# Kernel tuning notes

Hardware: AMD Instinct MI355X
Metric: run time of the kernel (lower is better)

## Reference

```python
import jax, jax.numpy as jnp
import numpy as np

# dims
N, K, M = 16000, 16, 20000      # nodes, neighbors per node, expanded (out-cell) nodes
C = 128                          # TP value channels = num_attn_heads * head_dim = scalar_dim
H = 8                            # num_attn_heads
LMAX = 2
L2 = (LMAX + 1) ** 2             # 9 spherical components
CE, CH = 64, 128                 # edge feature dim, radial MLP hidden
SD = 128                         # scalar_dim (irreps_node_input[0][0])


def _layer_norm(x, g, b, eps=1e-5):
    mu = jnp.mean(x, axis=-1, keepdims=True)
    var = jnp.var(x, axis=-1, keepdims=True)
    return (x - mu) * jax.lax.rsqrt(var + eps) * g + b


def setup_inputs() -> dict:
    key = jax.random.key(0)
    ks = jax.random.split(key, 20)
    f32 = jnp.float32
    return {
        "alpha": jax.random.normal(ks[0], (N, K, H), f32),
        "value": jax.random.normal(ks[1], (N, L2, C), f32) * 0.1,
        "x_edge": jax.random.normal(ks[2], (N, K, CE), f32),
        "node_pos": jax.random.normal(ks[3], (N, 3), f32) * 3.0,
        "edge_dis": jax.random.uniform(ks[4], (N, K), f32, 0.5, 4.5),
        "exp_node_pos": jax.random.normal(ks[5], (M, 3), f32) * 3.0,
        # radial MLP (RadialFunction: Linear -> LayerNorm -> SiLU -> Linear)
        "rad_w1": jax.random.normal(ks[6], (CE, CH), f32) / np.sqrt(CE),
        "rad_b1": jnp.zeros((CH,), f32),
        "ln_g": jnp.ones((CH,), f32),
        "ln_b": jnp.zeros((CH,), f32),
        "rad_w2": jax.random.normal(ks[7], (CH, SD), f32) / np.sqrt(CH),
        "rad_b2": jnp.zeros((SD,), f32),
        # uvw-connected first-order tensor-product weights (channel mixing per path)
        "tp_w_same": jax.random.normal(ks[8], (LMAX + 1, C, C), f32) / np.sqrt(C),
        "tp_w_rv0": jax.random.normal(ks[9], (C, C), f32) / np.sqrt(C),
        "tp_w_rdot": jax.random.normal(ks[10], (C, C), f32) / np.sqrt(C),
        # SO3 linear projection (per-degree linear, bias only on l=0)
        "proj_w": jax.random.normal(ks[11], (LMAX + 1, C, SD), f32) / np.sqrt(C),
        "proj_b": jnp.zeros((SD,), f32),
        # int index tensors
        "outcell_index": jax.random.randint(ks[12], (M,), 0, N, jnp.int32),
        "f_sparse_idx_expnode": jax.random.randint(ks[13], (N, K), 0, M, jnp.int32),
    }


def reference(alpha, value, x_edge, node_pos, edge_dis, exp_node_pos,
              rad_w1, rad_b1, ln_g, ln_b, rad_w2, rad_b2,
              tp_w_same, tp_w_rv0, tp_w_rdot, proj_w, proj_b,
              outcell_index, f_sparse_idx_expnode):
    # --- radial gating of attention weights ---
    h = jax.nn.silu(_layer_norm(x_edge @ rad_w1 + rad_b1, ln_g, ln_b))
    inputhead = h @ rad_w2 + rad_b2                          # [N,K,SD]
    n, k = alpha.shape[0], alpha.shape[1]
    a = alpha.reshape(n, k, H, 1) * inputhead.reshape(n, k, H, SD // H)
    a = a.reshape(n, k, SD)                                  # [N,K,C] (SD == C)
    a = a / (edge_dis[..., None] + 1e-8)

    # --- sparse equivariant first-order tensor product ---
    v_exp = value[outcell_index]                             # [M,L2,C]
    V = v_exp[f_sparse_idx_expnode]                          # [N,K,L2,C] (dominant gather)
    r = node_pos[:, None, :] - exp_node_pos[f_sparse_idx_expnode]  # [N,K,3]

    aV = jnp.einsum('nkc,nklc->nlc', a, V)                   # same-degree aggregation
    rv0 = a * V[:, :, 0, :]                                  # [N,K,C]
    arV0 = jnp.einsum('nkx,nkc->nxc', r, rv0)                # l=0 (x) r -> l=1
    wv1 = a[:, :, None, :] * V[:, :, 1:4, :]                 # [N,K,3,C]
    ardot = jnp.einsum('nkx,nkxc->nc', r, wv1)               # l=1 (x) r -> l=0

    out0 = aV[:, 0, :] @ tp_w_same[0] + ardot @ tp_w_rdot    # [N,C]
    out1 = jnp.einsum('nxc,cd->nxd', aV[:, 1:4, :], tp_w_same[1]) \
         + jnp.einsum('nxc,cd->nxd', arV0, tp_w_rv0)         # [N,3,C]
    out2 = jnp.einsum('nmc,cd->nmd', aV[:, 4:9, :], tp_w_same[2])  # [N,5,C]
    tp_out = jnp.concatenate([out0[:, None, :], out1, out2], axis=1)  # [N,9,C]

    # --- SO3 linear projection (per-degree) ---
    y0 = tp_out[:, 0, :] @ proj_w[0] + proj_b                # bias only on l=0
    y1 = jnp.einsum('nxc,cd->nxd', tp_out[:, 1:4, :], proj_w[1])
    y2 = jnp.einsum('nmc,cd->nmd', tp_out[:, 4:9, :], proj_w[2])
    return jnp.concatenate([y0[:, None, :], y1, y2], axis=1)  # [N,9,SD]
```

## Files before the change

### kernel.cpp

```cpp
#include <hip/hip_runtime.h>
#include <hip/hip_fp16.h>

typedef __attribute__((ext_vector_type(8))) short bh8;
typedef __attribute__((ext_vector_type(4))) float fv4;

#define NB 8
#define EB 128
#define BLK 512

#define MFMA(a, b, c) __builtin_amdgcn_mfma_f32_16x16x32_bf16((a), (b), (c), 0, 0, 0)

__device__ __forceinline__ unsigned short f2bf(float x) {
    unsigned int u = __float_as_uint(x);
    u += 0x7fffu + ((u >> 16) & 1u);
    return (unsigned short)(u >> 16);
}
__device__ __forceinline__ float bf2f(unsigned short h) {
    return __uint_as_float(((unsigned int)h) << 16);
}
__device__ __forceinline__ int swz(int row, int col) {
    return row * 128 + ((((col >> 3) ^ (row & 7)) << 3) | (col & 7));
}

__global__ void prep_kernel(
    const float* __restrict__ rad_w1, const float* __restrict__ rad_w2,
    const float* __restrict__ tp_w_same, const float* __restrict__ tp_w_rv0,
    const float* __restrict__ tp_w_rdot, const float* __restrict__ proj_w,
    unsigned short* __restrict__ ws)
{
    unsigned short* w1T = ws;
    unsigned short* w2T = ws + 8192;
    unsigned short* wcF = ws + 24576;
    const int b = blockIdx.x, t = threadIdx.x;
    if (b < 640) {
        const int m = b >> 7, d = b & 127;
        const float* A; const float* B;
        if (m == 0)      { A = tp_w_same;         B = proj_w; }
        else if (m == 1) { A = tp_w_rdot;         B = proj_w; }
        else if (m == 2) { A = tp_w_same + 16384; B = proj_w + 16384; }
        else if (m == 3) { A = tp_w_rv0;          B = proj_w + 16384; }
        else             { A = tp_w_same + 32768; B = proj_w + 32768; }
        __shared__ float Bs[128];
        Bs[t] = B[t * 128 + d];
        __syncthreads();
        float acc = 0.f;
        const float* Ar = A + t * 128;
        #pragma unroll 4
        for (int x = 0; x < 128; ++x) acc = fmaf(Ar[x], Bs[x], acc);
        const int wt = d >> 4, l15 = d & 15;
        const int ks = t >> 5, lq = (t & 31) >> 3, j = t & 7;
        const int lane = l15 + 16 * lq;
        wcF[(((m * 8 + wt) * 4 + ks) << 9) + lane * 8 + j] = f2bf(acc);
    } else {
        const int bb = b - 640;
        #pragma unroll
        for (int i = 0; i < 12; ++i) {
            const int idx = bb * 1536 + i * 128 + t;
            if (idx < 8192) {
                const int j = idx >> 6, c = idx & 63;
                w1T[idx] = f2bf(rad_w1[c * 128 + j]);
            } else if (idx < 24576) {
                const int i2 = idx - 8192;
                const int j = i2 >> 7, c = i2 & 127;
                w2T[i2] = f2bf(rad_w2[c * 128 + j]);
            }
        }
    }
}

__global__ __launch_bounds__(256) void conv_value_kernel(
    const float* __restrict__ v, unsigned short* __restrict__ o, int n8)
{
    const int i = blockIdx.x * 256 + threadIdx.x;
    if (i >= n8) return;
    const float4 a = *(const float4*)(v + (size_t)i * 8);
    const float4 b = *(const float4*)(v + (size_t)i * 8 + 4);
    uint4 r;
    r.x = (unsigned int)__half_as_ushort(__float2half_rn(a.x)) |
          ((unsigned int)__half_as_ushort(__float2half_rn(a.y)) << 16);
    r.y = (unsigned int)__half_as_ushort(__float2half_rn(a.z)) |
          ((unsigned int)__half_as_ushort(__float2half_rn(a.w)) << 16);
    r.z = (unsigned int)__half_as_ushort(__float2half_rn(b.x)) |
          ((unsigned int)__half_as_ushort(__float2half_rn(b.y)) << 16);
    r.w = (unsigned int)__half_as_ushort(__float2half_rn(b.z)) |
          ((unsigned int)__half_as_ushort(__float2half_rn(b.w)) << 16);
    *(uint4*)(o + (size_t)i * 8) = r;
}

template <int VHALF>
__global__ __launch_bounds__(BLK, 4) void foa_main(
    const float* __restrict__ alpha,
    const float* __restrict__ value,
    const float* __restrict__ x_edge,
    const float* __restrict__ node_pos,
    const float* __restrict__ edge_dis,
    const float* __restrict__ exp_node_pos,
    const float* __restrict__ rad_b1, const float* __restrict__ ln_g,
    const float* __restrict__ ln_b, const float* __restrict__ rad_b2,
    const float* __restrict__ proj_b,
    const unsigned short* __restrict__ ws,
    const unsigned short* __restrict__ vhf,
    const int* __restrict__ outcell_index,
    const int* __restrict__ f_sparse_idx,
    float* __restrict__ out)
{
    __shared__ __align__(16) unsigned short s_buf[16384];
    __shared__ __align__(16) unsigned short s_w2[16384];
    __shared__ float s_alpha[1024];
    __shared__ float s_rE[EB][3];
    __shared__ float s_invd[EB];
    __shared__ int   s_gidx[EB];

    const unsigned short* w1T = ws;
    const unsigned short* w2T = ws + 8192;
    const unsigned short* wcF = ws + 24576;

    const int t = threadIdx.x;
    const int e0 = blockIdx.x * EB;
    const int n0 = blockIdx.x * NB;
    const int lane = t & 63, w = t >> 6;
    const int ln15 = lane & 15, lq = lane >> 4;

    if (t < EB) {
        const int eidx = f_sparse_idx[e0 + t];
        s_gidx[t] = outcell_index[eidx];
        const int nn = n0 + (t >> 4);
        s_rE[t][0] = node_pos[nn * 3 + 0] - exp_node_pos[(size_t)eidx * 3 + 0];
        s_rE[t][1] = node_pos[nn * 3 + 1] - exp_node_pos[(size_t)eidx * 3 + 1];
        s_rE[t][2] = node_pos[nn * 3 + 2] - exp_node_pos[(size_t)eidx * 3 + 2];
        s_invd[t] = 1.0f / (edge_dis[e0 + t] + 1e-8f);
    }
    s_alpha[t]       = alpha[(size_t)e0 * 8 + t];
    s_alpha[t + 512] = alpha[(size_t)e0 * 8 + 512 + t];
    #pragma unroll
    for (int i = 0; i < 2; ++i) {
        const int chunk = i * BLK + t;
        const int row = chunk >> 3, grp = chunk & 7;
        const bh8 v = *(const bh8*)&w1T[row * 64 + grp * 8];
        *(bh8*)&s_w2[row * 64 + ((grp ^ (row & 7)) << 3)] = v;
    }
    __syncthreads();

    {
        bh8 af0, af1;
        {
            const float* xp = x_edge + ((size_t)(e0 + 16 * w + ln15)) * 64 + lq * 8;
            const float4 u0 = *(const float4*)(xp);
            const float4 u1 = *(const float4*)(xp + 4);
            const float4 u2 = *(const float4*)(xp + 32);
            const float4 u3 = *(const float4*)(xp + 36);
            af0[0] = (short)f2bf(u0.x); af0[1] = (short)f2bf(u0.y);
            af0[2] = (short)f2bf(u0.z); af0[3] = (short)f2bf(u0.w);
            af0[4] = (short)f2bf(u1.x); af0[5] = (short)f2bf(u1.y);
            af0[6] = (short)f2bf(u1.z); af0[7] = (short)f2bf(u1.w);
            af1[0] = (short)f2bf(u2.x); af1[1] = (short)f2bf(u2.y);
            af1[2] = (short)f2bf(u2.z); af1[3] = (short)f2bf(u2.w);
            af1[4] = (short)f2bf(u3.x); af1[5] = (short)f2bf(u3.y);
            af1[6] = (short)f2bf(u3.z); af1[7] = (short)f2bf(u3.w);
        }
        fv4 acc1[8];
        #pragma unroll
        for (int ct = 0; ct < 8; ++ct) { fv4 z = {0.f, 0.f, 0.f, 0.f}; acc1[ct] = z; }
        #pragma unroll
        for (int ct = 0; ct < 8; ++ct) {
            const int brow = 16 * ct + ln15;
            const bh8 b0 = *(const bh8*)&s_w2[brow * 64 + ((lq ^ (brow & 7)) << 3)];
            const bh8 b1 = *(const bh8*)&s_w2[brow * 64 + (((lq + 4) ^ (brow & 7)) << 3)];
            acc1[ct] = MFMA(af0, b0, acc1[ct]);
            acc1[ct] = MFMA(af1, b1, acc1[ct]);
        }
        float b1v[8], gv[8], bvv[8];
        #pragma unroll
        for (int ct = 0; ct < 8; ++ct) {
            b1v[ct] = rad_b1[16 * ct + ln15];
            gv[ct]  = ln_g[16 * ct + ln15];
            bvv[ct] = ln_b[16 * ct + ln15];
        }
        #pragma unroll
        for (int r = 0; r < 4; ++r) {
            float vv[8], s = 0.f, s2 = 0.f;
            #pragma unroll
            for (int ct = 0; ct < 8; ++ct) {
                const float x = acc1[ct][r] + b1v[ct];
                vv[ct] = x; s += x; s2 += x * x;
            }
            s += __shfl_xor(s, 1);  s2 += __shfl_xor(s2, 1);
            s += __shfl_xor(s, 2);  s2 += __shfl_xor(s2, 2);
            s += __shfl_xor(s, 4);  s2 += __shfl_xor(s2, 4);
            s += __shfl_xor(s, 8);  s2 += __shfl_xor(s2, 8);
            const float mu = s * 0.0078125f;
            const float var = s2 * 0.0078125f - mu * mu;
            const float rstd = rsqrtf(var + 1e-5f);
            const int rowg = 16 * w + lq * 4 + r;
            #pragma unroll
            for (int ct = 0; ct < 8; ++ct) {
                float hh = (vv[ct] - mu) * rstd * gv[ct] + bvv[ct];
                hh = hh / (1.f + __expf(-hh));
                s_buf[swz(rowg, 16 * ct + ln15)] = f2bf(hh);
            }
        }
    }
    __syncthreads();

    #pragma unroll
    for (int i = 0; i < 4; ++i) {
        const int chunk = i * BLK + t;
        const int row = chunk >> 4, grp = chunk & 15;
        const bh8 v = *(const bh8*)&w2T[row * 128 + grp * 8];
        *(bh8*)&s_w2[row * 128 + ((grp ^ (row & 7)) << 3)] = v;
    }
    __syncthreads();

    {
        bh8 afr[4];
        const int arow = 16 * w + ln15;
        #pragma unroll
        for (int ks = 0; ks < 4; ++ks) {
            const int acb = (lq + 4 * ks) ^ (arow & 7);
            afr[ks] = *(const bh8*)&s_buf[arow * 128 + (acb << 3)];
        }
        fv4 acc2[8];
        #pragma unroll
        for (int ct = 0; ct < 8; ++ct) { fv4 z = {0.f, 0.f, 0.f, 0.f}; acc2[ct] = z; }
        #pragma unroll
        for (int ks = 0; ks < 4; ++ks) {
            #pragma unroll
            for (int ct = 0; ct < 8; ++ct) {
                const int brow = 16 * ct + ln15;
                const bh8 b = *(const bh8*)&s_w2[brow * 128 +
                                  (((lq + 4 * ks) ^ (brow & 7)) << 3)];
                acc2[ct] = MFMA(afr[ks], b, acc2[ct]);
            }
        }
        #pragma unroll
        for (int ct = 0; ct < 8; ++ct) {
            const float b2 = rad_b2[16 * ct + ln15];
            #pragma unroll
            for (int r = 0; r < 4; ++r) {
                const int e = 16 * w + lq * 4 + r;
                const float aval = s_alpha[e * 8 + ct] * (acc2[ct][r] + b2) * s_invd[e];
                s_buf[swz(e, 16 * ct + ln15)] = f2bf(aval);
            }
        }
    }
    __syncthreads();

    const int c = t & 127;
    const int ng = t >> 7;
    float aV[9], arr[3], ard;

    #pragma unroll
    for (int ep = 0; ep < 2; ++ep) {
        #pragma unroll
        for (int l = 0; l < 9; ++l) aV[l] = 0.f;
        arr[0] = 0.f; arr[1] = 0.f; arr[2] = 0.f; ard = 0.f;
        #pragma unroll 4
        for (int k = 0; k < 16; ++k) {
            const int e = 32 * ng + 16 * ep + k;
            const float av = bf2f(s_buf[swz(e, c)]);
            float v0, v1, v2, v3, v4, v5, v6, v7, v8;
            if constexpr (VHALF) {
                const __half* vp = (const __half*)vhf + (size_t)s_gidx[e] * 1152 + c;
                v0 = __half2float(vp[0]);    v1 = __half2float(vp[128]);
                v2 = __half2float(vp[256]);  v3 = __half2float(vp[384]);
                v4 = __half2float(vp[512]);  v5 = __half2float(vp[640]);
                v6 = __half2float(vp[768]);  v7 = __half2float(vp[896]);
                v8 = __half2float(vp[1024]);
            } else {
                const float* vp = value + (size_t)s_gidx[e] * 1152 + c;
                v0 = vp[0];    v1 = vp[128];  v2 = vp[256];
                v3 = vp[384];  v4 = vp[512];  v5 = vp[640];
                v6 = vp[768];  v7 = vp[896];  v8 = vp[1024];
            }
            aV[0] = fmaf(av, v0, aV[0]); aV[1] = fmaf(av, v1, aV[1]);
            aV[2] = fmaf(av, v2, aV[2]); aV[3] = fmaf(av, v3, aV[3]);
            aV[4] = fmaf(av, v4, aV[4]); aV[5] = fmaf(av, v5, aV[5]);
            aV[6] = fmaf(av, v6, aV[6]); aV[7] = fmaf(av, v7, aV[7]);
            aV[8] = fmaf(av, v8, aV[8]);
            const float r0 = s_rE[e][0], r1 = s_rE[e][1], r2 = s_rE[e][2];
            const float w0 = av * v0;
            arr[0] = fmaf(r0, w0, arr[0]);
            arr[1] = fmaf(r1, w0, arr[1]);
            arr[2] = fmaf(r2, w0, arr[2]);
            ard = fmaf(av, fmaf(r0, v1, fmaf(r1, v2, r2 * v3)), ard);
        }
        __syncthreads();
        const int rb = 16 * ep;
        s_buf[swz(rb + 0  + ng, c)] = f2bf(aV[0]);
        s_buf[swz(rb + 4  + ng, c)] = f2bf(aV[1]);
        s_buf[swz(rb + 8  + ng, c)] = f2bf(aV[2]);
        s_buf[swz(rb + 12 + ng, c)] = f2bf(aV[3]);
        s_buf[swz(rb + 32 + ng, c)] = f2bf(ard);
        s_buf[swz(rb + 36 + ng, c)] = f2bf(arr[0]);
        s_buf[swz(rb + 40 + ng, c)] = f2bf(arr[1]);
        s_buf[swz(rb + 44 + ng, c)] = f2bf(arr[2]);
        s_buf[swz(rb + 64 + ng, c)] = f2bf(aV[4]);
        s_buf[swz(rb + 68 + ng, c)] = f2bf(aV[5]);
        s_buf[swz(rb + 72 + ng, c)] = f2bf(aV[6]);
        s_buf[swz(rb + 76 + ng, c)] = f2bf(aV[7]);
        s_buf[swz(96 + 4 * ep + ng, c)] = f2bf(aV[8]);
    }
    __syncthreads();

    {
        fv4 aEA, aEB, aEC, aOA, aOB, aOC, aG;
        { fv4 z = {0.f,0.f,0.f,0.f}; aEA=z; aEB=z; aEC=z; aOA=z; aOB=z; aOC=z; aG=z; }
        #pragma unroll
        for (int ks = 0; ks < 4; ++ks) {
            const int cb = lq + 4 * ks;
        #define LDA(tb) (*(const bh8*)&s_buf[((tb) + ln15) * 128 + (((cb) ^ (((tb) + ln15) & 7)) << 3)])
        #define LDB(m)  (*(const bh8*)&wcF[((((m) * 8 + w) * 4 + ks) << 9) + lane * 8])
            const bh8 W0 = LDB(0), Wd = LDB(1), W1 = LDB(2), Wr = LDB(3), W2 = LDB(4);
            const bh8 A0 = LDA(0),  A2 = LDA(32);
            aEA = MFMA(A0, W0, aEA);  aEA = MFMA(A2, Wd, aEA);
            aEB = MFMA(A0, W1, aEB);  aEB = MFMA(A2, Wr, aEB);
            const bh8 A1 = LDA(16), A3 = LDA(48);
            aOA = MFMA(A1, W0, aOA);  aOA = MFMA(A3, Wd, aOA);
            aOB = MFMA(A1, W1, aOB);  aOB = MFMA(A3, Wr, aOB);
            aEC = MFMA(LDA(64), W2, aEC);
            aOC = MFMA(LDA(80), W2, aOC);
            aG  = MFMA(LDA(96), W2, aG);
        #undef LDA
        #undef LDB
        }
        const int d = 16 * w + ln15;
        const float pb = proj_b[d];
        float* ob = out + (size_t)n0 * 1152 + d;
        #pragma unroll
        for (int r = 0; r < 4; ++r) {
            const int rt = lq * 4 + r;
            const int s = rt & 3;
            {
                const int l4 = 4 + (rt >> 2);
                ob[(size_t)(2 * s) * 1152 + l4 * 128]     = aEC[r];
                ob[(size_t)(2 * s + 1) * 1152 + l4 * 128] = aOC[r];
            }
            if (rt < 4) {
                ob[(size_t)(2 * rt) * 1152]             = aEA[r] + pb;
                ob[(size_t)(2 * rt + 1) * 1152]         = aOA[r] + pb;
                ob[(size_t)(2 * rt) * 1152 + 8 * 128]   = aG[r];
            } else {
                const int l = rt >> 2;
                ob[(size_t)(2 * s) * 1152 + l * 128]     = aEB[r];
                ob[(size_t)(2 * s + 1) * 1152 + l * 128] = aOB[r];
                if (rt < 8)
                    ob[(size_t)(2 * (rt - 4) + 1) * 1152 + 8 * 128] = aG[r];
            }
        }
    }
}

extern "C" void kernel_launch(void* const* d_in, const int* in_sizes, int n_in,
                              void* d_out, int out_size, void* d_ws, size_t ws_size,
                              hipStream_t stream)
{
    const float* alpha        = (const float*)d_in[0];
    const float* value        = (const float*)d_in[1];
    const float* x_edge       = (const float*)d_in[2];
    const float* node_pos     = (const float*)d_in[3];
    const float* edge_dis     = (const float*)d_in[4];
    const float* exp_node_pos = (const float*)d_in[5];
    const float* rad_w1       = (const float*)d_in[6];
    const float* rad_b1       = (const float*)d_in[7];
    const float* ln_g         = (const float*)d_in[8];
    const float* ln_b         = (const float*)d_in[9];
    const float* rad_w2       = (const float*)d_in[10];
    const float* rad_b2       = (const float*)d_in[11];
    const float* tp_w_same    = (const float*)d_in[12];
    const float* tp_w_rv0     = (const float*)d_in[13];
    const float* tp_w_rdot    = (const float*)d_in[14];
    const float* proj_w       = (const float*)d_in[15];
    const float* proj_b       = (const float*)d_in[16];
    const int* outcell_index  = (const int*)d_in[17];
    const int* f_sparse_idx   = (const int*)d_in[18];
    float* out = (float*)d_out;
    unsigned short* ws = (unsigned short*)d_ws;

    const int N = in_sizes[0] / (16 * 8);
    const int vElems = in_sizes[1];

    prep_kernel<<<656, 128, 0, stream>>>(rad_w1, rad_w2, tp_w_same, tp_w_rv0,
                                         tp_w_rdot, proj_w, ws);

    const size_t need = ((size_t)106496 + (size_t)vElems) * 2;
    if (ws_size >= need) {
        unsigned short* vhf = ws + 106496;
        const int n8 = vElems / 8;
        conv_value_kernel<<<(n8 + 255) / 256, 256, 0, stream>>>(value, vhf, n8);
        foa_main<1><<<N / NB, BLK, 0, stream>>>(alpha, value, x_edge, node_pos, edge_dis,
                                                exp_node_pos, rad_b1, ln_g, ln_b, rad_b2,
                                                proj_b, ws, vhf, outcell_index,
                                                f_sparse_idx, out);
    } else {
        foa_main<0><<<N / NB, BLK, 0, stream>>>(alpha, value, x_edge, node_pos, edge_dis,
                                                exp_node_pos, rad_b1, ln_g, ln_b, rad_b2,
                                                proj_b, ws, ws, outcell_index,
                                                f_sparse_idx, out);
    }
}
```

Before: 152.1 us.

## Pack fp16 value pairs into 32-bit words and hoist x_edge loads

The fp16 value conversion now interleaves pairs of spherical components per channel into 32-bit words, 640 words per node with the last component padded. The main kernel's gather then issues five loads per edge instead of nine and unpacks them with half2-to-float2 conversion. Separately, the x_edge fragment load and bf16 conversion are moved ahead of the shared-memory setup and the first barrier, so that global latency overlaps with the setup. The packed layout needs somewhat more workspace because of the padding, and the earlier load keeps those registers live longer.

```diff
diff --git a/kernel.cpp b/kernel.cpp
--- a/kernel.cpp
+++ b/kernel.cpp
@@ -68,23 +68,23 @@
     }
 }
 
-__global__ __launch_bounds__(256) void conv_value_kernel(
-    const float* __restrict__ v, unsigned short* __restrict__ o, int n8)
+__global__ __launch_bounds__(128) void conv_value_p_kernel(
+    const float* __restrict__ v, unsigned int* __restrict__ o)
 {
-    const int i = blockIdx.x * 256 + threadIdx.x;
-    if (i >= n8) return;
-    const float4 a = *(const float4*)(v + (size_t)i * 8);
-    const float4 b = *(const float4*)(v + (size_t)i * 8 + 4);
-    uint4 r;
-    r.x = (unsigned int)__half_as_ushort(__float2half_rn(a.x)) |
-          ((unsigned int)__half_as_ushort(__float2half_rn(a.y)) << 16);
-    r.y = (unsigned int)__half_as_ushort(__float2half_rn(a.z)) |
-          ((unsigned int)__half_as_ushort(__float2half_rn(a.w)) << 16);
-    r.z = (unsigned int)__half_as_ushort(__float2half_rn(b.x)) |
-          ((unsigned int)__half_as_ushort(__float2half_rn(b.y)) << 16);
-    r.w = (unsigned int)__half_as_ushort(__float2half_rn(b.z)) |
-          ((unsigned int)__half_as_ushort(__float2half_rn(b.w)) << 16);
-    *(uint4*)(o + (size_t)i * 8) = r;
+    const int n = blockIdx.x;
+    const int c = threadIdx.x;
+    const float* vp = v + (size_t)n * 1152 + c;
+    float x[9];
+    #pragma unroll
+    for (int l = 0; l < 9; ++l) x[l] = vp[l * 128];
+    unsigned int* op = o + (size_t)n * 640 + c;
+    #pragma unroll
+    for (int lp = 0; lp < 4; ++lp) {
+        const unsigned int lo = __half_as_ushort(__float2half_rn(x[2 * lp]));
+        const unsigned int hi = __half_as_ushort(__float2half_rn(x[2 * lp + 1]));
+        op[lp * 128] = lo | (hi << 16);
+    }
+    op[512] = (unsigned int)__half_as_ushort(__float2half_rn(x[8]));
 }
 
 template <int VHALF>
@@ -99,7 +99,7 @@
     const float* __restrict__ ln_b, const float* __restrict__ rad_b2,
     const float* __restrict__ proj_b,
     const unsigned short* __restrict__ ws,
-    const unsigned short* __restrict__ vhf,
+    const unsigned int* __restrict__ vhp,
     const int* __restrict__ outcell_index,
     const int* __restrict__ f_sparse_idx,
     float* __restrict__ out)
@@ -121,6 +121,22 @@
     const int lane = t & 63, w = t >> 6;
     const int ln15 = lane & 15, lq = lane >> 4;
 
+    bh8 af0, af1;
+    {
+        const float* xp = x_edge + ((size_t)(e0 + 16 * w + ln15)) * 64 + lq * 8;
+        const float4 u0 = *(const float4*)(xp);
+        const float4 u1 = *(const float4*)(xp + 4);
+        const float4 u2 = *(const float4*)(xp + 32);
+        const float4 u3 = *(const float4*)(xp + 36);
+        af0[0] = (short)f2bf(u0.x); af0[1] = (short)f2bf(u0.y);
+        af0[2] = (short)f2bf(u0.z); af0[3] = (short)f2bf(u0.w);
+        af0[4] = (short)f2bf(u1.x); af0[5] = (short)f2bf(u1.y);
+        af0[6] = (short)f2bf(u1.z); af0[7] = (short)f2bf(u1.w);
+        af1[0] = (short)f2bf(u2.x); af1[1] = (short)f2bf(u2.y);
+        af1[2] = (short)f2bf(u2.z); af1[3] = (short)f2bf(u2.w);
+        af1[4] = (short)f2bf(u3.x); af1[5] = (short)f2bf(u3.y);
+        af1[6] = (short)f2bf(u3.z); af1[7] = (short)f2bf(u3.w);
+    }
     if (t < EB) {
         const int eidx = f_sparse_idx[e0 + t];
         s_gidx[t] = outcell_index[eidx];
@@ -142,22 +158,6 @@
     __syncthreads();
 
     {
-        bh8 af0, af1;
-        {
-            const float* xp = x_edge + ((size_t)(e0 + 16 * w + ln15)) * 64 + lq * 8;
-            const float4 u0 = *(const float4*)(xp);
-            const float4 u1 = *(const float4*)(xp + 4);
-            const float4 u2 = *(const float4*)(xp + 32);
-            const float4 u3 = *(const float4*)(xp + 36);
-            af0[0] = (short)f2bf(u0.x); af0[1] = (short)f2bf(u0.y);
-            af0[2] = (short)f2bf(u0.z); af0[3] = (short)f2bf(u0.w);
-            af0[4] = (short)f2bf(u1.x); af0[5] = (short)f2bf(u1.y);
-            af0[6] = (short)f2bf(u1.z); af0[7] = (short)f2bf(u1.w);
-            af1[0] = (short)f2bf(u2.x); af1[1] = (short)f2bf(u2.y);
-            af1[2] = (short)f2bf(u2.z); af1[3] = (short)f2bf(u2.w);
-            af1[4] = (short)f2bf(u3.x); af1[5] = (short)f2bf(u3.y);
-            af1[6] = (short)f2bf(u3.z); af1[7] = (short)f2bf(u3.w);
-        }
         fv4 acc1[8];
         #pragma unroll
         for (int ct = 0; ct < 8; ++ct) { fv4 z = {0.f, 0.f, 0.f, 0.f}; acc1[ct] = z; }
@@ -260,12 +260,19 @@
             const float av = bf2f(s_buf[swz(e, c)]);
             float v0, v1, v2, v3, v4, v5, v6, v7, v8;
             if constexpr (VHALF) {
-                const __half* vp = (const __half*)vhf + (size_t)s_gidx[e] * 1152 + c;
-                v0 = __half2float(vp[0]);    v1 = __half2float(vp[128]);
-                v2 = __half2float(vp[256]);  v3 = __half2float(vp[384]);
-                v4 = __half2float(vp[512]);  v5 = __half2float(vp[640]);
-                v6 = __half2float(vp[768]);  v7 = __half2float(vp[896]);
-                v8 = __half2float(vp[1024]);
+                const unsigned int* vp = vhp + (size_t)s_gidx[e] * 640 + c;
+                const unsigned int q0 = vp[0];
+                const unsigned int q1 = vp[128];
+                const unsigned int q2 = vp[256];
+                const unsigned int q3 = vp[384];
+                const unsigned short q4 = *(const unsigned short*)(vp + 512);
+                const float2 f0 = __half22float2(*(const __half2*)&q0);
+                const float2 f1 = __half22float2(*(const __half2*)&q1);
+                const float2 f2 = __half22float2(*(const __half2*)&q2);
+                const float2 f3 = __half22float2(*(const __half2*)&q3);
+                v0 = f0.x; v1 = f0.y; v2 = f1.x; v3 = f1.y;
+                v4 = f2.x; v5 = f2.y; v6 = f3.x; v7 = f3.y;
+                v8 = __half2float(__ushort_as_half(q4));
             } else {
                 const float* vp = value + (size_t)s_gidx[e] * 1152 + c;
                 v0 = vp[0];    v1 = vp[128];  v2 = vp[256];
@@ -378,23 +385,23 @@
 
     const int N = in_sizes[0] / (16 * 8);
     const int vElems = in_sizes[1];
+    const int vN = vElems / 1152;
 
     prep_kernel<<<656, 128, 0, stream>>>(rad_w1, rad_w2, tp_w_same, tp_w_rv0,
                                          tp_w_rdot, proj_w, ws);
 
-    const size_t need = ((size_t)106496 + (size_t)vElems) * 2;
+    const size_t need = ((size_t)106496 + (size_t)vN * 1280) * 2;
     if (ws_size >= need) {
-        unsigned short* vhf = ws + 106496;
-        const int n8 = vElems / 8;
-        conv_value_kernel<<<(n8 + 255) / 256, 256, 0, stream>>>(value, vhf, n8);
+        unsigned int* vhp = (unsigned int*)(ws + 106496);
+        conv_value_p_kernel<<<vN, 128, 0, stream>>>(value, vhp);
         foa_main<1><<<N / NB, BLK, 0, stream>>>(alpha, value, x_edge, node_pos, edge_dis,
                                                 exp_node_pos, rad_b1, ln_g, ln_b, rad_b2,
-                                                proj_b, ws, vhf, outcell_index,
+                                                proj_b, ws, vhp, outcell_index,
                                                 f_sparse_idx, out);
     } else {
         foa_main<0><<<N / NB, BLK, 0, stream>>>(alpha, value, x_edge, node_pos, edge_dis,
                                                 exp_node_pos, rad_b1, ln_g, ln_b, rad_b2,
-                                                proj_b, ws, ws, outcell_index,
-                                                f_sparse_idx, out);
-    }
-}
+                                                proj_b, ws, (const unsigned int*)ws,
+                                                outcell_index, f_sparse_idx, out);
+    }
+}
```

Result: slower. 162.0 us (+6.5%).
